# Kernel tuning notes

Measured on AMD Instinct MI355X. Metric: run time of the kernel, lower is better.

## Reference

```python
import jax, jax.numpy as jnp
import numpy as np

N_NODES = 50000
N_EDGES = 500000
D = 128          # n_features
HID = 64         # explainer MLP hidden dim
TEMP = 5.0       # temp[0], epoch-0 temperature
SAMPLE_BIAS = 0.0


def setup_inputs() -> dict:
    key = jax.random.key(0)
    ks = jax.random.split(key, 8)
    embeds = jax.random.normal(ks[0], (N_NODES, D), dtype=jnp.float32)
    W1 = jax.random.normal(ks[1], (3 * D, HID), dtype=jnp.float32) * 0.05
    b1 = jnp.zeros((HID,), dtype=jnp.float32)
    W2 = jax.random.normal(ks[2], (HID, 1), dtype=jnp.float32) * 0.05
    b2 = jnp.zeros((1,), dtype=jnp.float32)
    u = jax.random.uniform(ks[3], (N_EDGES, 1), dtype=jnp.float32)
    src = jax.random.randint(ks[4], (N_EDGES,), 0, N_NODES, dtype=jnp.int64 if jax.config.jax_enable_x64 else jnp.int32)
    dst = jax.random.randint(ks[5], (N_EDGES,), 0, N_NODES, dtype=jnp.int64 if jax.config.jax_enable_x64 else jnp.int32)
    n = 0  # target node index within the subgraph
    return {"embeds": embeds, "W1": W1, "b1": b1, "W2": W2, "b2": b2,
            "u": u, "src": src, "dst": dst, "n": n}


def reference(embeds, W1, b1, W2, b2, u, src, dst, n):
    # --- _create_explainer_input: edge-wise gather + concat with target node embed ---
    row_embeds = embeds[src]                                   # [E, D]
    col_embeds = embeds[dst]                                   # [E, D]
    node_data = jnp.broadcast_to(embeds[n][None, :], row_embeds.shape)  # [E, D]
    inputs = jnp.concatenate([row_embeds, col_embeds, node_data], axis=1)  # [E, 3D]
    # --- explainer_model: Linear(3D,64) -> ReLU -> Linear(64,1) ---
    h = jax.nn.relu(inputs @ W1 + b1)                          # [E, HID]
    sampling_weights = h @ W2 + b2                             # [E, 1]
    # --- _sample_graph (training=True): Gumbel-sigmoid ---
    bias = SAMPLE_BIAS + 0.0001
    eps = (bias - (1.0 - bias)) * u + (1.0 - bias)             # U(bias, 1-bias)
    gate_inputs = jnp.log(eps) - jnp.log1p(-eps)
    mask = jax.nn.sigmoid((gate_inputs + sampling_weights) / TEMP)
    return mask.squeeze(-1)                                    # [E]
```

## Files before the change

### kernel.cpp

```cpp
#include <hip/hip_runtime.h>
#include <hip/hip_bf16.h>
#include <string.h>


#define D 128
#define HID 64

typedef __attribute__((ext_vector_type(8))) short short8;
typedef __attribute__((ext_vector_type(4))) float f32x4;
typedef _Float16 h2 __attribute__((ext_vector_type(2)));

union U32H2 { unsigned u; h2 h; };

__device__ inline unsigned short f2bf(float f) {
    union { float f; unsigned int u; } x;
    x.f = f;
    unsigned int r = x.u + 0x7FFFu + ((x.u >> 16) & 1u);
    return (unsigned short)(r >> 16);
}

__device__ inline unsigned int f2e5u(float f) {
    _Float16 h = (_Float16)f;
    unsigned short u;
    __builtin_memcpy(&u, &h, 2);
    unsigned short r = (unsigned short)(u + 0x7Fu + ((u >> 8) & 1u));
    return (unsigned int)(r >> 8) & 0xFFu;
}

__device__ inline unsigned packh(float lo, float hi) {
    _Float16 l = (_Float16)lo, h = (_Float16)hi;
    unsigned short ul, uh;
    __builtin_memcpy(&ul, &l, 2);
    __builtin_memcpy(&uh, &h, 2);
    return (unsigned)ul | ((unsigned)uh << 16);
}

__device__ inline h2 relu2(h2 x) {
#if __has_builtin(__builtin_elementwise_max)
    return __builtin_elementwise_max(x, (h2)((_Float16)0));
#else
    h2 r;
    r[0] = x[0] > (_Float16)0 ? x[0] : (_Float16)0;
    r[1] = x[1] > (_Float16)0 ? x[1] : (_Float16)0;
    return r;
#endif
}

__device__ inline float dot2acc(h2 a, h2 b, float c) {
#if __has_builtin(__builtin_amdgcn_fdot2)
    return __builtin_amdgcn_fdot2(a, b, c, false);
#else
    c = fmaf((float)a[0], (float)b[0], c);
    return fmaf((float)a[1], (float)b[1], c);
#endif
}

__global__ __launch_bounds__(256) void pg_prep(
    const float* __restrict__ embeds, const float* __restrict__ W1,
    const float* __restrict__ b1, const float* __restrict__ W2,
    const int* __restrict__ nidx,
    unsigned short* __restrict__ bfrag,
    unsigned* __restrict__ cnodeh, unsigned* __restrict__ w2h)
{
    int t = threadIdx.x;
    if (blockIdx.x < 64) {
        int i    = blockIdx.x * 256 + t;
        int j    = i & 7;
        int lane = (i >> 3) & 63;
        int ct   = (i >> 9) & 7;
        int ks   = i >> 12;
        int k    = ks * 32 + (lane >> 4) * 8 + j;
        int col  = ct * 16 + (lane & 15);
        float w  = (col < HID) ? W1[k * HID + col]
                               : W1[(D + k) * HID + (col - HID)];
        bfrag[i] = f2bf(w);
    } else {
        __shared__ float cs[HID];
        if (t < HID) {
            int n = nidx[0];
            const float* nr = embeds + (size_t)n * D;
            float c = b1[t];
            #pragma unroll 8
            for (int k = 0; k < D; ++k)
                c = fmaf(nr[k], W1[(2 * D + k) * HID + t], c);
            cs[t] = c;
        }
        __syncthreads();
        if (t < 32) {
            int wi = t >> 1, sub = t & 1;
            int j = 4 * wi + sub;
            cnodeh[t] = packh(cs[j], cs[j + 2]);
            w2h[t]    = packh(W2[j], W2[j + 2]);
        }
    }
}

__global__ __launch_bounds__(256) void pg_nodes(
    const float* __restrict__ embeds, const unsigned short* __restrict__ bfrag,
    unsigned char* __restrict__ P, int N, int NTILES)
{
    __shared__ unsigned char st[4][16 * 144];

    int wave  = threadIdx.x >> 6;
    int lane  = threadIdx.x & 63;
    int ntile = blockIdx.x * 4 + wave;
    if (ntile >= NTILES) return;

    int kg = lane >> 4;
    int nr = ntile * 16 + (lane & 15);
    if (nr >= N) nr = N - 1;
    const float* row = embeds + (size_t)nr * D + kg * 8;

    short8 af[4];
    #pragma unroll
    for (int ks = 0; ks < 4; ++ks) {
        float4 v0 = *reinterpret_cast<const float4*>(row + ks * 32);
        float4 v1 = *reinterpret_cast<const float4*>(row + ks * 32 + 4);
        union { float f; unsigned u; } c[8];
        c[0].f = v0.x; c[1].f = v0.y; c[2].f = v0.z; c[3].f = v0.w;
        c[4].f = v1.x; c[5].f = v1.y; c[6].f = v1.z; c[7].f = v1.w;
        union { unsigned u[4]; short8 s; } pk;
        #pragma unroll
        for (int p = 0; p < 4; ++p)
            pk.u[p] = (c[2 * p + 1].u & 0xFFFF0000u) | (c[2 * p].u >> 16);
        af[ks] = pk.s;
    }

    const short8* gw = reinterpret_cast<const short8*>(bfrag);

    f32x4 acc[8];
    #pragma unroll
    for (int ct = 0; ct < 8; ++ct) acc[ct] = (f32x4){0.f, 0.f, 0.f, 0.f};

    #pragma unroll
    for (int ct = 0; ct < 8; ++ct) {
        #pragma unroll
        for (int ks = 0; ks < 4; ++ks) {
            short8 wf = gw[(ks * 8 + ct) * 64 + lane];
            acc[ct] = __builtin_amdgcn_mfma_f32_16x16x32_bf16(wf, af[ks], acc[ct], 0, 0, 0);
        }
    }

    #pragma unroll
    for (int ct = 0; ct < 8; ++ct) {
        unsigned w = f2e5u(acc[ct][0])
                   | (f2e5u(acc[ct][1]) << 8)
                   | (f2e5u(acc[ct][2]) << 16)
                   | (f2e5u(acc[ct][3]) << 24);
        *reinterpret_cast<unsigned*>(&st[wave][(lane & 15) * 144 + ct * 16 + kg * 4]) = w;
    }
    #pragma unroll
    for (int h = 0; h < 2; ++h) {
        int c   = lane + h * 64;
        int r   = c >> 3;
        int off = (c & 7) * 16;
        uint4 v = *reinterpret_cast<const uint4*>(&st[wave][r * 144 + off]);
        int node = ntile * 16 + r;
        if (node < N)
            *reinterpret_cast<uint4*>(P + (size_t)node * 128 + off) = v;
    }
}

__device__ inline float mlp_sw(const uint4 A[4], const uint4 B[4],
                               const unsigned* __restrict__ cn,
                               const unsigned* __restrict__ w2, float sw)
{
    #pragma unroll
    for (int g = 0; g < 4; ++g) {
        unsigned aw[4] = {A[g].x, A[g].y, A[g].z, A[g].w};
        unsigned bw[4] = {B[g].x, B[g].y, B[g].z, B[g].w};
        #pragma unroll
        for (int w = 0; w < 4; ++w) {
            int wi = g * 4 + w;
            U32H2 a0, a1, b0, b1, c0, c1, W0, W1v;
            a0.u = (aw[w] << 8) & 0xFF00FF00u;
            a1.u =  aw[w]       & 0xFF00FF00u;
            b0.u = (bw[w] << 8) & 0xFF00FF00u;
            b1.u =  bw[w]       & 0xFF00FF00u;
            c0.u = cn[2 * wi];     c1.u = cn[2 * wi + 1];
            W0.u = w2[2 * wi];     W1v.u = w2[2 * wi + 1];
            h2 h0 = relu2(a0.h + b0.h + c0.h);
            h2 h1 = relu2(a1.h + b1.h + c1.h);
            sw = dot2acc(h0, W0.h, sw);
            sw = dot2acc(h1, W1v.h, sw);
        }
    }
    return sw;
}

__device__ inline float gumbel_sigmoid(float uu, float sw) {
    float a = 0.9999f - 0.9998f * uu;
    float b = 0.0001f + 0.9998f * uu;
    float gate = __logf(__fdividef(a, b));
    float x = (gate + sw) * 0.2f;
    return __fdividef(1.f, 1.f + __expf(-x));
}

__global__ __launch_bounds__(256) void pg_edge(
    const unsigned char* __restrict__ P,
    const unsigned* __restrict__ cnodeh, const unsigned* __restrict__ w2h,
    const float* __restrict__ b2, const float* __restrict__ u,
    const int* __restrict__ src, const int* __restrict__ dst,
    float* __restrict__ out, int E)
{
    int p  = blockIdx.x * 256 + threadIdx.x;
    int e0 = p * 2;
    if (e0 >= E) return;
    bool two = (e0 + 1 < E);

    int s0, s1, d0, d1;
    float u0, u1;
    if (two) {
        int2 sv = *reinterpret_cast<const int2*>(src + e0);
        int2 dv = *reinterpret_cast<const int2*>(dst + e0);
        float2 uv = *reinterpret_cast<const float2*>(u + e0);
        s0 = sv.x; s1 = sv.y; d0 = dv.x; d1 = dv.y; u0 = uv.x; u1 = uv.y;
    } else {
        s0 = s1 = src[e0]; d0 = d1 = dst[e0]; u0 = u1 = u[e0];
    }

    const uint4* ra0 = reinterpret_cast<const uint4*>(P + (size_t)s0 * 128);
    const uint4* rb0 = reinterpret_cast<const uint4*>(P + (size_t)d0 * 128 + 64);
    const uint4* ra1 = reinterpret_cast<const uint4*>(P + (size_t)s1 * 128);
    const uint4* rb1 = reinterpret_cast<const uint4*>(P + (size_t)d1 * 128 + 64);

    uint4 A0[4], B0[4], A1[4], B1[4];
    #pragma unroll
    for (int g = 0; g < 4; ++g) { A0[g] = ra0[g]; B0[g] = rb0[g]; }
    #pragma unroll
    for (int g = 0; g < 4; ++g) { A1[g] = ra1[g]; B1[g] = rb1[g]; }

    float swi = b2[0];
    float sw0 = mlp_sw(A0, B0, cnodeh, w2h, swi);
    float sw1 = mlp_sw(A1, B1, cnodeh, w2h, swi);

    float m0 = gumbel_sigmoid(u0, sw0);
    float m1 = gumbel_sigmoid(u1, sw1);

    if (two) {
        float2 o = {m0, m1};
        *reinterpret_cast<float2*>(out + e0) = o;
    } else {
        out[e0] = m0;
    }
}

extern "C" void kernel_launch(void* const* d_in, const int* in_sizes, int n_in,
                              void* d_out, int out_size, void* d_ws, size_t ws_size,
                              hipStream_t stream) {
    const float* embeds = (const float*)d_in[0];
    const float* W1     = (const float*)d_in[1];
    const float* b1     = (const float*)d_in[2];
    const float* W2     = (const float*)d_in[3];
    const float* b2     = (const float*)d_in[4];
    const float* u      = (const float*)d_in[5];
    const int*   src    = (const int*)d_in[6];
    const int*   dst    = (const int*)d_in[7];
    const int*   nidx   = (const int*)d_in[8];

    int E = in_sizes[6];
    int N = in_sizes[0] / D;
    int NTILES = (N + 15) / 16;

    unsigned short* bfrag = (unsigned short*)d_ws;
    unsigned* cnodeh = (unsigned*)(bfrag + 16384);
    unsigned* w2h    = cnodeh + 32;
    unsigned char* P = (unsigned char*)(w2h + 32);

    pg_prep<<<65, 256, 0, stream>>>(embeds, W1, b1, W2, nidx, bfrag, cnodeh, w2h);
    pg_nodes<<<(NTILES + 3) / 4, 256, 0, stream>>>(embeds, bfrag, P, N, NTILES);

    int pairs = (E + 1) / 2;
    pg_edge<<<(pairs + 255) / 256, 256, 0, stream>>>(P, cnodeh, w2h, b2, u,
                                                     src, dst, (float*)d_out, E);
}
```

Baseline: 42.12 us.

## Split each edge pair's hidden-dim MLP across four lanes with shuffle reduction

New measurement: 36.67 us. -12.9%, faster.

```diff
diff --git a/kernel.cpp b/kernel.cpp
--- a/kernel.cpp
+++ b/kernel.cpp
@@ -161,29 +161,25 @@
     }
 }
 
-__device__ inline float mlp_sw(const uint4 A[4], const uint4 B[4],
-                               const unsigned* __restrict__ cn,
-                               const unsigned* __restrict__ w2, float sw)
-{
-    #pragma unroll
-    for (int g = 0; g < 4; ++g) {
-        unsigned aw[4] = {A[g].x, A[g].y, A[g].z, A[g].w};
-        unsigned bw[4] = {B[g].x, B[g].y, B[g].z, B[g].w};
-        #pragma unroll
-        for (int w = 0; w < 4; ++w) {
-            int wi = g * 4 + w;
-            U32H2 a0, a1, b0, b1, c0, c1, W0, W1v;
-            a0.u = (aw[w] << 8) & 0xFF00FF00u;
-            a1.u =  aw[w]       & 0xFF00FF00u;
-            b0.u = (bw[w] << 8) & 0xFF00FF00u;
-            b1.u =  bw[w]       & 0xFF00FF00u;
-            c0.u = cn[2 * wi];     c1.u = cn[2 * wi + 1];
-            W0.u = w2[2 * wi];     W1v.u = w2[2 * wi + 1];
-            h2 h0 = relu2(a0.h + b0.h + c0.h);
-            h2 h1 = relu2(a1.h + b1.h + c1.h);
-            sw = dot2acc(h0, W0.h, sw);
-            sw = dot2acc(h1, W1v.h, sw);
-        }
+__device__ inline float mlp16(uint4 A, uint4 B,
+                              const unsigned* cnv, const unsigned* w2v)
+{
+    float sw = 0.f;
+    unsigned aw[4] = {A.x, A.y, A.z, A.w};
+    unsigned bw[4] = {B.x, B.y, B.z, B.w};
+    #pragma unroll
+    for (int w = 0; w < 4; ++w) {
+        U32H2 a0, a1, b0, b1, c0, c1, W0, W1v;
+        a0.u = (aw[w] << 8) & 0xFF00FF00u;
+        a1.u =  aw[w]       & 0xFF00FF00u;
+        b0.u = (bw[w] << 8) & 0xFF00FF00u;
+        b1.u =  bw[w]       & 0xFF00FF00u;
+        c0.u = cnv[2 * w];  c1.u = cnv[2 * w + 1];
+        W0.u = w2v[2 * w];  W1v.u = w2v[2 * w + 1];
+        h2 h0 = relu2(a0.h + b0.h + c0.h);
+        h2 h1 = relu2(a1.h + b1.h + c1.h);
+        sw = dot2acc(h0, W0.h, sw);
+        sw = dot2acc(h1, W1v.h, sw);
     }
     return sw;
 }
@@ -203,45 +199,53 @@
     const int* __restrict__ src, const int* __restrict__ dst,
     float* __restrict__ out, int E)
 {
-    int p  = blockIdx.x * 256 + threadIdx.x;
-    int e0 = p * 2;
+    int r    = threadIdx.x & 3;
+    int quad = (blockIdx.x * 256 + threadIdx.x) >> 2;
+    int e0   = quad * 2;
     if (e0 >= E) return;
     bool two = (e0 + 1 < E);
 
-    int s0, s1, d0, d1;
-    float u0, u1;
+    unsigned cnv[8], w2v[8];
+    #pragma unroll
+    for (int w = 0; w < 4; ++w) {
+        int wi = 4 * r + w;
+        cnv[2 * w]     = cnodeh[2 * wi];
+        cnv[2 * w + 1] = cnodeh[2 * wi + 1];
+        w2v[2 * w]     = w2h[2 * wi];
+        w2v[2 * w + 1] = w2h[2 * wi + 1];
+    }
+
+    int2 sv, dv;
     if (two) {
-        int2 sv = *reinterpret_cast<const int2*>(src + e0);
-        int2 dv = *reinterpret_cast<const int2*>(dst + e0);
-        float2 uv = *reinterpret_cast<const float2*>(u + e0);
-        s0 = sv.x; s1 = sv.y; d0 = dv.x; d1 = dv.y; u0 = uv.x; u1 = uv.y;
+        sv = *reinterpret_cast<const int2*>(src + e0);
+        dv = *reinterpret_cast<const int2*>(dst + e0);
     } else {
-        s0 = s1 = src[e0]; d0 = d1 = dst[e0]; u0 = u1 = u[e0];
-    }
-
-    const uint4* ra0 = reinterpret_cast<const uint4*>(P + (size_t)s0 * 128);
-    const uint4* rb0 = reinterpret_cast<const uint4*>(P + (size_t)d0 * 128 + 64);
-    const uint4* ra1 = reinterpret_cast<const uint4*>(P + (size_t)s1 * 128);
-    const uint4* rb1 = reinterpret_cast<const uint4*>(P + (size_t)d1 * 128 + 64);
-
-    uint4 A0[4], B0[4], A1[4], B1[4];
-    #pragma unroll
-    for (int g = 0; g < 4; ++g) { A0[g] = ra0[g]; B0[g] = rb0[g]; }
-    #pragma unroll
-    for (int g = 0; g < 4; ++g) { A1[g] = ra1[g]; B1[g] = rb1[g]; }
-
-    float swi = b2[0];
-    float sw0 = mlp_sw(A0, B0, cnodeh, w2h, swi);
-    float sw1 = mlp_sw(A1, B1, cnodeh, w2h, swi);
-
-    float m0 = gumbel_sigmoid(u0, sw0);
-    float m1 = gumbel_sigmoid(u1, sw1);
-
-    if (two) {
-        float2 o = {m0, m1};
-        *reinterpret_cast<float2*>(out + e0) = o;
-    } else {
-        out[e0] = m0;
+        sv.x = sv.y = src[e0];
+        dv.x = dv.y = dst[e0];
+    }
+
+    uint4 A0 = *reinterpret_cast<const uint4*>(P + (size_t)sv.x * 128 + r * 16);
+    uint4 B0 = *reinterpret_cast<const uint4*>(P + (size_t)dv.x * 128 + 64 + r * 16);
+    uint4 A1 = *reinterpret_cast<const uint4*>(P + (size_t)sv.y * 128 + r * 16);
+    uint4 B1 = *reinterpret_cast<const uint4*>(P + (size_t)dv.y * 128 + 64 + r * 16);
+
+    float sw0 = mlp16(A0, B0, cnv, w2v);
+    float sw1 = mlp16(A1, B1, cnv, w2v);
+
+    sw0 += __shfl_xor(sw0, 1); sw0 += __shfl_xor(sw0, 2);
+    sw1 += __shfl_xor(sw1, 1); sw1 += __shfl_xor(sw1, 2);
+
+    if (r == 0) {
+        float bb = b2[0];
+        if (two) {
+            float2 uv = *reinterpret_cast<const float2*>(u + e0);
+            float2 o;
+            o.x = gumbel_sigmoid(uv.x, sw0 + bb);
+            o.y = gumbel_sigmoid(uv.y, sw1 + bb);
+            *reinterpret_cast<float2*>(out + e0) = o;
+        } else {
+            out[e0] = gumbel_sigmoid(u[e0], sw0 + bb);
+        }
     }
 }
 
@@ -270,7 +274,8 @@
     pg_prep<<<65, 256, 0, stream>>>(embeds, W1, b1, W2, nidx, bfrag, cnodeh, w2h);
     pg_nodes<<<(NTILES + 3) / 4, 256, 0, stream>>>(embeds, bfrag, P, N, NTILES);
 
-    int pairs = (E + 1) / 2;
-    pg_edge<<<(pairs + 255) / 256, 256, 0, stream>>>(P, cnodeh, w2h, b2, u,
-                                                     src, dst, (float*)d_out, E);
-}
+    long threads = ((long)E + 1) / 2 * 4;
+    int blocks = (int)((threads + 255) / 256);
+    pg_edge<<<blocks, 256, 0, stream>>>(P, cnodeh, w2h, b2, u,
+                                        src, dst, (float*)d_out, E);
+}
```
